# Performance work log

Measured on AMD Instinct MI355X. Metric: run time of the kernel, lower is better.

Reference implementation:

```python
import jax, jax.numpy as jnp
import numpy as np
import math

B, T, C, H = 2, 2048, 1024, 16
HD = C // H
WINDOW = 256  # local_attn_ctx with attnblocksize=1


def setup_inputs() -> dict:
    key = jax.random.key(0)
    k1, k2, k3 = jax.random.split(key, 3)
    x = jax.random.normal(k1, (B, T, C), dtype=jnp.float32)
    Wqkv = jax.random.normal(k2, (C, 3 * C), dtype=jnp.float32) * 0.02
    bqkv = jnp.zeros((3 * C,), dtype=jnp.float32)
    Wproj = jax.random.normal(k3, (C, C), dtype=jnp.float32) * 0.02
    bproj = jnp.zeros((C,), dtype=jnp.float32)
    # 'local' block-sparse layout at token granularity: causal + sliding window
    i = np.arange(T)[:, None]
    j = np.arange(T)[None, :]
    mask = ((j <= i) & (i - j <= WINDOW)).astype(np.int32)
    return {"x": x, "Wqkv": Wqkv, "bqkv": bqkv, "Wproj": Wproj, "bproj": bproj,
            "mask": jnp.asarray(mask)}


def reference(x, Wqkv, bqkv, Wproj, bproj, mask):
    Bb, Tt, Cc = x.shape
    qkv = (x @ Wqkv + bqkv).reshape(Bb, Tt, 3, H, HD)  # [B,T,3,H,hd]
    q = jnp.transpose(qkv[:, :, 0], (0, 2, 1, 3))  # [B,H,T,hd]
    k = jnp.transpose(qkv[:, :, 1], (0, 2, 1, 3))
    v = jnp.transpose(qkv[:, :, 2], (0, 2, 1, 3))
    scale = 1.0 / math.sqrt(HD)
    att = jnp.einsum('bhqd,bhkd->bhqk', q, k) * scale  # dense T x T scores
    att = jnp.where(mask[:Tt, :Tt] == 0, -jnp.inf, att)
    att = jax.nn.softmax(att, axis=-1)
    y = jnp.einsum('bhqk,bhkd->bhqd', att, v)
    y = jnp.transpose(y, (0, 2, 1, 3)).reshape(Bb, Tt, Cc)
    return y @ Wproj + bproj
```

## Files before the change

### kernel.cpp

```cpp
#include <hip/hip_runtime.h>
#include <hip/hip_bf16.h>
#include <math.h>

typedef __bf16 bf16;
typedef __attribute__((ext_vector_type(8))) __bf16 bf16x8;
typedef __attribute__((ext_vector_type(4))) __bf16 bf16x4;
typedef __attribute__((ext_vector_type(4))) float f32x4;

#define B_  2
#define T_  2048
#define C_  1024
#define H_  16
#define HD_ 64
#define WIN_ 256

#define GLOAD16(g, l)                                                        \
  __builtin_amdgcn_global_load_lds(                                          \
      (const __attribute__((address_space(1))) void*)(g),                    \
      (__attribute__((address_space(3))) void*)(l), 16, 0, 0)

__device__ inline void bar() {
  asm volatile("" ::: "memory");
  __builtin_amdgcn_s_barrier();
  asm volatile("" ::: "memory");
}


__global__ __launch_bounds__(256) void prologue_k(const float* __restrict__ x,
                                                  bf16* __restrict__ xb,
                                                  const float* __restrict__ Wqkv,
                                                  bf16* __restrict__ wqkvT,
                                                  const float* __restrict__ Wproj,
                                                  bf16* __restrict__ wprojT) {
  __shared__ float t[32][33];
  const int blk = blockIdx.x;
  const int tid = threadIdx.x;

  if (blk < 4096) {
    const int idx = blk * 256 + tid;
    const float4 v = ((const float4*)x)[idx];
    bf16x4 o;
    o[0] = (bf16)v.x; o[1] = (bf16)v.y; o[2] = (bf16)v.z; o[3] = (bf16)v.w;
    ((bf16x4*)xb)[idx] = o;
    return;
  }

  const float* W; bf16* WT; int N, tb;
  if (blk < 4096 + 3072) { tb = blk - 4096; W = Wqkv;  WT = wqkvT;  N = 3 * C_; }
  else                   { tb = blk - 7168; W = Wproj; WT = wprojT; N = C_;     }
  const int xt = N / 32;
  const int n0 = (tb % xt) * 32, k0 = (tb / xt) * 32;
  const int tx = tid & 31, ty = tid >> 5;

  #pragma unroll
  for (int i = 0; i < 32; i += 8)
    t[ty + i][tx] = W[(size_t)(k0 + ty + i) * N + (n0 + tx)];
  __syncthreads();
  #pragma unroll
  for (int i = 0; i < 32; i += 8)
    WT[(size_t)(n0 + ty + i) * C_ + (k0 + tx)] = (bf16)t[tx][ty + i];
}


template <int TM, int TN, int WM, int WN, int MINW, int MODE>
__global__ __launch_bounds__(WM * WN * 64, MINW)
void gemm_db_k(const bf16* __restrict__ A, const bf16* __restrict__ Bt,
               const float* __restrict__ bias,
               void* __restrict__ out0, void* __restrict__ out1,
               int M, int N, int K) {
  constexpr int NW    = WM * WN;
  constexpr int WROWS = TM / WM;
  constexpr int WCOLS = TN / WN;
  constexpr int FM    = WROWS / 16;
  constexpr int FN    = WCOLS / 16;
  constexpr int NCH   = (TM + TN) / 8;
  constexpr int CPW   = NCH / NW;

  const int bm = blockIdx.x * TM;
  const int bn = blockIdx.y * TN;
  const int tid  = threadIdx.x;
  const int wid  = tid >> 6;
  const int lane = tid & 63;
  const int wr = wid / WN;
  const int wc = wid % WN;
  const int lr = lane & 15;
  const int g  = lane >> 4;

  __shared__ bf16 As[2][TM * 64];
  __shared__ bf16 Bs[2][TN * 64];

  f32x4 acc[FM][FN] = {};

  const int sr = lane >> 3;
  const int sc = ((lane & 7) ^ sr) << 3;

  #define STG(p_, u_)                                                        \
    do {                                                                     \
      _Pragma("unroll")                                                      \
      for (int i = 0; i < CPW; ++i) {                                        \
        const int c = wid * CPW + i;                                         \
        if (c < TM / 8) {                                                    \
          GLOAD16(A + (size_t)(bm + c * 8 + sr) * K + (u_) * 64 + sc,        \
                  &As[p_][c * 8 * 64]);                                      \
        } else {                                                             \
          GLOAD16(Bt + (size_t)(bn + (c - TM / 8) * 8 + sr) * K + (u_) * 64 + sc, \
                  &Bs[p_][(c - TM / 8) * 8 * 64]);                           \
        }                                                                    \
      }                                                                      \
    } while (0)

  const int NT = K >> 6;
  const int kc0 = ((0 + g) ^ (lr & 7)) << 3;
  const int kc1 = ((4 + g) ^ (lr & 7)) << 3;

  STG(0, 0);
  asm volatile("s_waitcnt vmcnt(0)" ::: "memory");
  __builtin_amdgcn_s_barrier();
  asm volatile("" ::: "memory");

  for (int u = 0; u < NT; ++u) {
    const int p = u & 1;
    if (u + 1 < NT) {
      STG(p ^ 1, u + 1);
      asm volatile("s_waitcnt vmcnt(%0)" :: "i"(CPW) : "memory");
    } else {
      asm volatile("s_waitcnt vmcnt(0)" ::: "memory");
    }
    bar();

    const bf16* Ar = &As[p][(wr * WROWS + lr) * 64];
    const bf16* Br = &Bs[p][(wc * WCOLS + lr) * 64];
    #pragma unroll
    for (int s = 0; s < 2; ++s) {
      const int kc = s ? kc1 : kc0;
      bf16x8 av[FM], bvv[FN];
      #pragma unroll
      for (int m = 0; m < FM; ++m)
        av[m] = *(const bf16x8*)(Ar + m * 16 * 64 + kc);
      #pragma unroll
      for (int n = 0; n < FN; ++n)
        bvv[n] = *(const bf16x8*)(Br + n * 16 * 64 + kc);
      __builtin_amdgcn_s_setprio(1);
      #pragma unroll
      for (int m = 0; m < FM; ++m)
        #pragma unroll
        for (int n = 0; n < FN; ++n)
          acc[m][n] = __builtin_amdgcn_mfma_f32_16x16x32_bf16(av[m], bvv[n], acc[m][n], 0, 0, 0);
      __builtin_amdgcn_s_setprio(0);
    }
    bar();
  }
  #undef STG

  const int orow = g * 4;
  #pragma unroll
  for (int n = 0; n < FN; ++n) {
    const int nbase = bn + wc * WCOLS + n * 16;
    const int gn = nbase + lr;
    const float bv_ = bias[gn];
    #pragma unroll
    for (int m = 0; m < FM; ++m) {
      const int gm0 = bm + wr * WROWS + m * 16 + orow;
      if (MODE == 0) {
        #pragma unroll
        for (int r = 0; r < 4; ++r)
          ((float*)out0)[(size_t)(gm0 + r) * N + gn] = acc[m][n][r] + bv_;
      } else {
        if (nbase < 2 * C_) {
          #pragma unroll
          for (int r = 0; r < 4; ++r)
            ((bf16*)out0)[(size_t)(gm0 + r) * (2 * C_) + gn] = (bf16)(acc[m][n][r] + bv_);
        } else {
          const int vcol = gn - 2 * C_;
          const int h = vcol >> 6, d = vcol & 63;
          const int b = gm0 >> 11, tok = gm0 & (T_ - 1);
          bf16x4 o;
          #pragma unroll
          for (int r = 0; r < 4; ++r) o[r] = (bf16)(acc[m][n][r] + bv_);
          *(bf16x4*)&((bf16*)out1)[(((size_t)b * H_ + h) * HD_ + d) * T_ + tok] = o;
        }
      }
    }
  }
}


__global__ __launch_bounds__(256) void attn_mfma_k(const bf16* __restrict__ qk,
                                                   const bf16* __restrict__ vt,
                                                   bf16* __restrict__ y) {
  const int q0 = blockIdx.x * 64;
  const int h  = blockIdx.y;
  const int b  = blockIdx.z;
  const int tid  = threadIdx.x;
  const int wid  = tid >> 6;
  const int lane = tid & 63;
  const int lr = lane & 15;
  const int g  = lane >> 4;

  __shared__ bf16 Ks[64 * 64];
  __shared__ bf16 Vs[64 * 64];
  __shared__ bf16 Ps[4][16][72];

  const int qrow = q0 + wid * 16 + lr;
  const bf16* qptr = qk + ((size_t)(b * T_ + qrow)) * (2 * C_) + h * HD_;
  bf16x8 qf[2];
  qf[0] = *(const bf16x8*)(qptr + g * 8);
  qf[1] = *(const bf16x8*)(qptr + 32 + g * 8);

  float m = -1e30f, l = 0.f;
  f32x4 yacc[4] = {};

  const int sr = lane >> 3;
  const int sc = ((lane & 7) ^ sr) << 3;
  const int kc0 = ((0 + g) ^ (lr & 7)) << 3;
  const int kc1 = ((4 + g) ^ (lr & 7)) << 3;

  const int kt_lo = (blockIdx.x >= 4) ? (int)blockIdx.x - 4 : 0;
  for (int kt = kt_lo; kt <= (int)blockIdx.x; ++kt) {
    #pragma unroll
    for (int i = 0; i < 2; ++i) {
      const int c = wid * 2 + i;
      GLOAD16(qk + ((size_t)(b * T_) + kt * 64 + c * 8 + sr) * (2 * C_) + C_ + h * HD_ + sc,
              &Ks[c * 8 * 64]);
      GLOAD16(vt + (((size_t)b * H_ + h) * HD_ + c * 8 + sr) * T_ + kt * 64 + sc,
              &Vs[c * 8 * 64]);
    }
    asm volatile("s_waitcnt vmcnt(0)" ::: "memory");
    bar();

    f32x4 sacc[4] = {};
    __builtin_amdgcn_s_setprio(1);
    #pragma unroll
    for (int t = 0; t < 4; ++t) {
      sacc[t] = __builtin_amdgcn_mfma_f32_16x16x32_bf16(
          *(const bf16x8*)&Ks[(t * 16 + lr) * 64 + kc0], qf[0], sacc[t], 0, 0, 0);
      sacc[t] = __builtin_amdgcn_mfma_f32_16x16x32_bf16(
          *(const bf16x8*)&Ks[(t * 16 + lr) * 64 + kc1], qf[1], sacc[t], 0, 0, 0);
    }
    __builtin_amdgcn_s_setprio(0);

    float pv[4][4];
    float rmax = -1e30f;
    #pragma unroll
    for (int t = 0; t < 4; ++t)
      #pragma unroll
      for (int r = 0; r < 4; ++r) {
        const int key = kt * 64 + t * 16 + g * 4 + r;
        const bool valid = (key <= qrow) && (qrow - key <= WIN_);
        const float sv = valid ? sacc[t][r] * 0.125f : -__builtin_inff();
        pv[t][r] = sv;
        rmax = fmaxf(rmax, sv);
      }
    rmax = fmaxf(rmax, __shfl_xor(rmax, 16));
    rmax = fmaxf(rmax, __shfl_xor(rmax, 32));

    const float mnew = fmaxf(m, rmax);
    const float alpha = __expf(m - mnew);
    m = mnew;
    float lsum = 0.f;
    #pragma unroll
    for (int t = 0; t < 4; ++t)
      #pragma unroll
      for (int r = 0; r < 4; ++r) {
        const float e = __expf(pv[t][r] - mnew);
        pv[t][r] = e;
        lsum += e;
      }
    lsum += __shfl_xor(lsum, 16);
    lsum += __shfl_xor(lsum, 32);
    l = l * alpha + lsum;

    #pragma unroll
    for (int t = 0; t < 4; ++t) {
      bf16x4 pk;
      #pragma unroll
      for (int r = 0; r < 4; ++r) pk[r] = (bf16)pv[t][r];
      *(bf16x4*)&Ps[wid][lr][t * 16 + g * 4] = pk;
    }

    float al[4];
    #pragma unroll
    for (int r = 0; r < 4; ++r) al[r] = __shfl(alpha, g * 4 + r);
    #pragma unroll
    for (int t = 0; t < 4; ++t)
      #pragma unroll
      for (int r = 0; r < 4; ++r) yacc[t][r] *= al[r];

    bf16x8 pf[2];
    pf[0] = *(const bf16x8*)&Ps[wid][lr][g * 8];
    pf[1] = *(const bf16x8*)&Ps[wid][lr][32 + g * 8];
    __builtin_amdgcn_s_setprio(1);
    #pragma unroll
    for (int t = 0; t < 4; ++t) {
      yacc[t] = __builtin_amdgcn_mfma_f32_16x16x32_bf16(
          pf[0], *(const bf16x8*)&Vs[(t * 16 + lr) * 64 + kc0], yacc[t], 0, 0, 0);
      yacc[t] = __builtin_amdgcn_mfma_f32_16x16x32_bf16(
          pf[1], *(const bf16x8*)&Vs[(t * 16 + lr) * 64 + kc1], yacc[t], 0, 0, 0);
    }
    __builtin_amdgcn_s_setprio(0);
    bar();
  }

  float li[4];
  #pragma unroll
  for (int r = 0; r < 4; ++r) li[r] = 1.f / __shfl(l, g * 4 + r);
  #pragma unroll
  for (int t = 0; t < 4; ++t)
    #pragma unroll
    for (int r = 0; r < 4; ++r) {
      const int tok = q0 + wid * 16 + g * 4 + r;
      y[((size_t)(b * T_ + tok)) * C_ + h * HD_ + t * 16 + lr] = (bf16)(yacc[t][r] * li[r]);
    }
}


extern "C" void kernel_launch(void* const* d_in, const int* in_sizes, int n_in,
                              void* d_out, int out_size, void* d_ws, size_t ws_size,
                              hipStream_t stream) {
  const float* x     = (const float*)d_in[0];
  const float* Wqkv  = (const float*)d_in[1];
  const float* bqkv  = (const float*)d_in[2];
  const float* Wproj = (const float*)d_in[3];
  const float* bproj = (const float*)d_in[4];
  float* out = (float*)d_out;

  const size_t SZ_QK  = (size_t)B_ * T_ * 2 * C_ * sizeof(bf16);
  const size_t SZ_VT  = (size_t)B_ * H_ * HD_ * T_ * sizeof(bf16);
  const size_t SZ_XB  = (size_t)B_ * T_ * C_ * sizeof(bf16);
  const size_t SZ_WQT = (size_t)3 * C_ * C_ * sizeof(bf16);
  const size_t SZ_WPT = (size_t)C_ * C_ * sizeof(bf16);
  const size_t NEED   = SZ_QK + SZ_VT + SZ_XB + SZ_WQT + SZ_WPT + SZ_XB;
  if (ws_size < NEED) return;

  char* ws = (char*)d_ws;
  bf16* qkb    = (bf16*)(ws);
  bf16* vtb    = (bf16*)(ws + SZ_QK);
  bf16* xb     = (bf16*)(ws + SZ_QK + SZ_VT);
  bf16* wqkvT  = (bf16*)(ws + SZ_QK + SZ_VT + SZ_XB);
  bf16* wprojT = (bf16*)(ws + SZ_QK + SZ_VT + SZ_XB + SZ_WQT);
  bf16* yb     = (bf16*)(ws + SZ_QK + SZ_VT + SZ_XB + SZ_WQT + SZ_WPT);

  prologue_k<<<8192, 256, 0, stream>>>(x, xb, Wqkv, wqkvT, Wproj, wprojT);

  gemm_db_k<128, 192, 2, 4, 4, 2><<<dim3((B_ * T_) / 128, (3 * C_) / 192), 512, 0, stream>>>(
      xb, wqkvT, bqkv, qkb, vtb, B_ * T_, 3 * C_, C_);

  attn_mfma_k<<<dim3(T_ / 64, H_, B_), 256, 0, stream>>>(qkb, vtb, yb);

  gemm_db_k<64, 128, 2, 2, 2, 0><<<dim3((B_ * T_) / 64, C_ / 128), 256, 0, stream>>>(
      yb, wprojT, bproj, out, nullptr, B_ * T_, C_, C_);
}
```

Baseline: 81.53 us.

## Double-buffer K/V tiles in attention with 128-query blocks and per-wave tile skipping

The attention kernel now handles 128 queries per block with 8 waves, so each staged K/V tile is reused by twice as many query rows. The next tile is prefetched into a second LDS buffer while the current one is computed. Each wave skips MFMA and softmax work for key tiles that fall entirely outside its causal window. In exchange there are half as many blocks (512), more LDS per block, and a loop that spans 6 tiles with warps idle on skipped tiles.

Result: no change. 80.25 us (median of 2 runs) (-1.6%).

```diff
diff --git a/kernel.cpp b/kernel.cpp
--- a/kernel.cpp
+++ b/kernel.cpp
@@ -185,10 +185,10 @@
 }
 
 
-__global__ __launch_bounds__(256) void attn_mfma_k(const bf16* __restrict__ qk,
-                                                   const bf16* __restrict__ vt,
-                                                   bf16* __restrict__ y) {
-  const int q0 = blockIdx.x * 64;
+__global__ __launch_bounds__(512) void attn_mfma2_k(const bf16* __restrict__ qk,
+                                                    const bf16* __restrict__ vt,
+                                                    bf16* __restrict__ y) {
+  const int q0 = blockIdx.x * 128;
   const int h  = blockIdx.y;
   const int b  = blockIdx.z;
   const int tid  = threadIdx.x;
@@ -197,109 +197,133 @@
   const int lr = lane & 15;
   const int g  = lane >> 4;
 
-  __shared__ bf16 Ks[64 * 64];
-  __shared__ bf16 Vs[64 * 64];
-  __shared__ bf16 Ps[4][16][72];
+  __shared__ bf16 Ks[2][64 * 64];
+  __shared__ bf16 Vs[2][64 * 64];
+  __shared__ bf16 Ps[8][16][72];
 
   const int qrow = q0 + wid * 16 + lr;
   const bf16* qptr = qk + ((size_t)(b * T_ + qrow)) * (2 * C_) + h * HD_;
-  bf16x8 qf[2];
-  qf[0] = *(const bf16x8*)(qptr + g * 8);
-  qf[1] = *(const bf16x8*)(qptr + 32 + g * 8);
+  bf16x8 qf0 = *(const bf16x8*)(qptr + g * 8);
+  bf16x8 qf1 = *(const bf16x8*)(qptr + 32 + g * 8);
 
   float m = -1e30f, l = 0.f;
   f32x4 yacc[4] = {};
+
+  const int bx = blockIdx.x;
+  const int kt_lo = (bx * 2 >= 4) ? bx * 2 - 4 : 0;
+  const int kt_hi = bx * 2 + 1;
 
   const int sr = lane >> 3;
   const int sc = ((lane & 7) ^ sr) << 3;
   const int kc0 = ((0 + g) ^ (lr & 7)) << 3;
   const int kc1 = ((4 + g) ^ (lr & 7)) << 3;
 
-  const int kt_lo = (blockIdx.x >= 4) ? (int)blockIdx.x - 4 : 0;
-  for (int kt = kt_lo; kt <= (int)blockIdx.x; ++kt) {
-    #pragma unroll
-    for (int i = 0; i < 2; ++i) {
-      const int c = wid * 2 + i;
-      GLOAD16(qk + ((size_t)(b * T_) + kt * 64 + c * 8 + sr) * (2 * C_) + C_ + h * HD_ + sc,
-              &Ks[c * 8 * 64]);
-      GLOAD16(vt + (((size_t)b * H_ + h) * HD_ + c * 8 + sr) * T_ + kt * 64 + sc,
-              &Vs[c * 8 * 64]);
-    }
-    asm volatile("s_waitcnt vmcnt(0)" ::: "memory");
+  #define STAGEKV(p_, kt_)                                                     \
+    do {                                                                       \
+      _Pragma("unroll")                                                        \
+      for (int i = 0; i < 2; ++i) {                                            \
+        const int c = wid * 2 + i;                                             \
+        if (c < 8)                                                             \
+          GLOAD16(qk + ((size_t)(b * T_) + (kt_) * 64 + c * 8 + sr) * (2 * C_) \
+                       + C_ + h * HD_ + sc,                                    \
+                  &Ks[p_][c * 8 * 64]);                                        \
+        else                                                                   \
+          GLOAD16(vt + (((size_t)b * H_ + h) * HD_ + (c - 8) * 8 + sr) * T_    \
+                       + (kt_) * 64 + sc,                                      \
+                  &Vs[p_][(c - 8) * 8 * 64]);                                  \
+      }                                                                        \
+    } while (0)
+
+  STAGEKV(0, kt_lo);
+  asm volatile("s_waitcnt vmcnt(0)" ::: "memory");
+  bar();
+
+  for (int kt = kt_lo; kt <= kt_hi; ++kt) {
+    const int idx = kt - kt_lo;
+    const int p   = idx & 1;
+    if (kt + 1 <= kt_hi) {
+      STAGEKV(p ^ 1, kt + 1);
+      asm volatile("s_waitcnt vmcnt(2)" ::: "memory");
+    } else {
+      asm volatile("s_waitcnt vmcnt(0)" ::: "memory");
+    }
     bar();
 
-    f32x4 sacc[4] = {};
-    __builtin_amdgcn_s_setprio(1);
-    #pragma unroll
-    for (int t = 0; t < 4; ++t) {
-      sacc[t] = __builtin_amdgcn_mfma_f32_16x16x32_bf16(
-          *(const bf16x8*)&Ks[(t * 16 + lr) * 64 + kc0], qf[0], sacc[t], 0, 0, 0);
-      sacc[t] = __builtin_amdgcn_mfma_f32_16x16x32_bf16(
-          *(const bf16x8*)&Ks[(t * 16 + lr) * 64 + kc1], qf[1], sacc[t], 0, 0, 0);
-    }
-    __builtin_amdgcn_s_setprio(0);
-
-    float pv[4][4];
-    float rmax = -1e30f;
-    #pragma unroll
-    for (int t = 0; t < 4; ++t)
-      #pragma unroll
-      for (int r = 0; r < 4; ++r) {
-        const int key = kt * 64 + t * 16 + g * 4 + r;
-        const bool valid = (key <= qrow) && (qrow - key <= WIN_);
-        const float sv = valid ? sacc[t][r] * 0.125f : -__builtin_inff();
-        pv[t][r] = sv;
-        rmax = fmaxf(rmax, sv);
+    const int wq = q0 + wid * 16;
+    if (kt * 64 <= wq + 15 && kt * 64 + 63 >= wq - WIN_) {
+      f32x4 sacc[4] = {};
+      __builtin_amdgcn_s_setprio(1);
+      #pragma unroll
+      for (int t = 0; t < 4; ++t) {
+        sacc[t] = __builtin_amdgcn_mfma_f32_16x16x32_bf16(
+            *(const bf16x8*)&Ks[p][(t * 16 + lr) * 64 + kc0], qf0, sacc[t], 0, 0, 0);
+        sacc[t] = __builtin_amdgcn_mfma_f32_16x16x32_bf16(
+            *(const bf16x8*)&Ks[p][(t * 16 + lr) * 64 + kc1], qf1, sacc[t], 0, 0, 0);
       }
-    rmax = fmaxf(rmax, __shfl_xor(rmax, 16));
-    rmax = fmaxf(rmax, __shfl_xor(rmax, 32));
-
-    const float mnew = fmaxf(m, rmax);
-    const float alpha = __expf(m - mnew);
-    m = mnew;
-    float lsum = 0.f;
-    #pragma unroll
-    for (int t = 0; t < 4; ++t)
-      #pragma unroll
-      for (int r = 0; r < 4; ++r) {
-        const float e = __expf(pv[t][r] - mnew);
-        pv[t][r] = e;
-        lsum += e;
+      __builtin_amdgcn_s_setprio(0);
+
+      float pv[4][4];
+      float rmax = -1e30f;
+      #pragma unroll
+      for (int t = 0; t < 4; ++t)
+        #pragma unroll
+        for (int r = 0; r < 4; ++r) {
+          const int key = kt * 64 + t * 16 + g * 4 + r;
+          const bool valid = (key <= qrow) && (qrow - key <= WIN_);
+          const float sv = valid ? sacc[t][r] * 0.125f : -__builtin_inff();
+          pv[t][r] = sv;
+          rmax = fmaxf(rmax, sv);
+        }
+      rmax = fmaxf(rmax, __shfl_xor(rmax, 16));
+      rmax = fmaxf(rmax, __shfl_xor(rmax, 32));
+
+      const float mnew = fmaxf(m, rmax);
+      const float alpha = __expf(m - mnew);
+      m = mnew;
+      float lsum = 0.f;
+      #pragma unroll
+      for (int t = 0; t < 4; ++t)
+        #pragma unroll
+        for (int r = 0; r < 4; ++r) {
+          const float e = __expf(pv[t][r] - mnew);
+          pv[t][r] = e;
+          lsum += e;
+        }
+      lsum += __shfl_xor(lsum, 16);
+      lsum += __shfl_xor(lsum, 32);
+      l = l * alpha + lsum;
+
+      #pragma unroll
+      for (int t = 0; t < 4; ++t) {
+        bf16x4 pk;
+        #pragma unroll
+        for (int r = 0; r < 4; ++r) pk[r] = (bf16)pv[t][r];
+        *(bf16x4*)&Ps[wid][lr][t * 16 + g * 4] = pk;
       }
-    lsum += __shfl_xor(lsum, 16);
-    lsum += __shfl_xor(lsum, 32);
-    l = l * alpha + lsum;
-
-    #pragma unroll
-    for (int t = 0; t < 4; ++t) {
-      bf16x4 pk;
-      #pragma unroll
-      for (int r = 0; r < 4; ++r) pk[r] = (bf16)pv[t][r];
-      *(bf16x4*)&Ps[wid][lr][t * 16 + g * 4] = pk;
-    }
-
-    float al[4];
-    #pragma unroll
-    for (int r = 0; r < 4; ++r) al[r] = __shfl(alpha, g * 4 + r);
-    #pragma unroll
-    for (int t = 0; t < 4; ++t)
-      #pragma unroll
-      for (int r = 0; r < 4; ++r) yacc[t][r] *= al[r];
-
-    bf16x8 pf[2];
-    pf[0] = *(const bf16x8*)&Ps[wid][lr][g * 8];
-    pf[1] = *(const bf16x8*)&Ps[wid][lr][32 + g * 8];
-    __builtin_amdgcn_s_setprio(1);
-    #pragma unroll
-    for (int t = 0; t < 4; ++t) {
-      yacc[t] = __builtin_amdgcn_mfma_f32_16x16x32_bf16(
-          pf[0], *(const bf16x8*)&Vs[(t * 16 + lr) * 64 + kc0], yacc[t], 0, 0, 0);
-      yacc[t] = __builtin_amdgcn_mfma_f32_16x16x32_bf16(
-          pf[1], *(const bf16x8*)&Vs[(t * 16 + lr) * 64 + kc1], yacc[t], 0, 0, 0);
-    }
-    __builtin_amdgcn_s_setprio(0);
+
+      float al[4];
+      #pragma unroll
+      for (int r = 0; r < 4; ++r) al[r] = __shfl(alpha, g * 4 + r);
+      #pragma unroll
+      for (int t = 0; t < 4; ++t)
+        #pragma unroll
+        for (int r = 0; r < 4; ++r) yacc[t][r] *= al[r];
+
+      bf16x8 pf0 = *(const bf16x8*)&Ps[wid][lr][g * 8];
+      bf16x8 pf1 = *(const bf16x8*)&Ps[wid][lr][32 + g * 8];
+      __builtin_amdgcn_s_setprio(1);
+      #pragma unroll
+      for (int t = 0; t < 4; ++t) {
+        yacc[t] = __builtin_amdgcn_mfma_f32_16x16x32_bf16(
+            pf0, *(const bf16x8*)&Vs[p][(t * 16 + lr) * 64 + kc0], yacc[t], 0, 0, 0);
+        yacc[t] = __builtin_amdgcn_mfma_f32_16x16x32_bf16(
+            pf1, *(const bf16x8*)&Vs[p][(t * 16 + lr) * 64 + kc1], yacc[t], 0, 0, 0);
+      }
+      __builtin_amdgcn_s_setprio(0);
+    }
     bar();
   }
+  #undef STAGEKV
 
   float li[4];
   #pragma unroll
@@ -345,7 +369,7 @@
   gemm_db_k<128, 192, 2, 4, 4, 2><<<dim3((B_ * T_) / 128, (3 * C_) / 192), 512, 0, stream>>>(
       xb, wqkvT, bqkv, qkb, vtb, B_ * T_, 3 * C_, C_);
 
-  attn_mfma_k<<<dim3(T_ / 64, H_, B_), 256, 0, stream>>>(qkb, vtb, yb);
+  attn_mfma2_k<<<dim3(T_ / 128, H_, B_), 512, 0, stream>>>(qkb, vtb, yb);
 
   gemm_db_k<64, 128, 2, 2, 2, 0><<<dim3((B_ * T_) / 64, C_ / 128), 256, 0, stream>>>(
       yb, wprojT, bproj, out, nullptr, B_ * T_, C_, C_);
```
